# Kernel optimization log

Hardware: AMD Instinct MI355X
Metric: run time of the kernel (lower is better)

The kernel has to match this reference:

```python
import jax, jax.numpy as jnp
import numpy as np

B, Q, K, D, H, HD, HID, ED, CPB, E = 2, 300, 1024, 256, 8, 32, 32, 256, 256, 131072
N = B * Q
EPS = 1e-5


def _ln(x, g, b):
    mu = x.mean(-1, keepdims=True)
    v = ((x - mu) ** 2).mean(-1, keepdims=True)
    return (x - mu) / jnp.sqrt(v + EPS) * g + b


def setup_inputs():
    key = jax.random.key(0)
    ks = jax.random.split(key, 32)
    rn = lambda k, s, sc=0.02: jax.random.normal(k, s, jnp.float32) * sc
    return {
        "nodes": jax.random.normal(ks[0], (N, D), jnp.float32),
        "images": jax.random.normal(ks[1], (B, K, D), jnp.float32),
        "rel_coords": jax.random.normal(ks[2], (B, Q, K, 2), jnp.float32),
        "edge_feats": jax.random.normal(ks[3], (E, ED), jnp.float32),
        "edge_index": jax.random.randint(ks[4], (2, E), 0, N, jnp.int32),
        "images_mask": jnp.zeros((B, K), dtype=bool),
        "ln1_g": jnp.ones((D,)), "ln1_b": jnp.zeros((D,)),
        "ln2_g": jnp.ones((D,)), "ln2_b": jnp.zeros((D,)),
        "ln3_g": jnp.ones((D,)), "ln3_b": jnp.zeros((D,)),
        "Wni": rn(ks[5], (D, HID * H)), "bni": jnp.zeros((HID * H,)),
        "Wnj": rn(ks[6], (D, HID * H)), "bnj": jnp.zeros((HID * H,)),
        "We": rn(ks[7], (ED, HID * H)), "be": jnp.zeros((HID * H,)),
        "attn_proj": jax.random.normal(ks[8], (H, HID), jnp.float32),
        "Wmsg": rn(ks[9], (D + ED, D)), "bmsg": jnp.zeros((D,)),
        "Wg_out": rn(ks[10], (D, D)), "bg_out": jnp.zeros((D,)),
        "Wq": rn(ks[11], (D, D)), "bq": jnp.zeros((D,)),
        "Wkv": rn(ks[12], (D, 2 * D)), "bkv": jnp.zeros((2 * D,)),
        "Wc1": rn(ks[13], (2, CPB), 0.5), "bc1": jnp.zeros((CPB,)),
        "Wc2": rn(ks[14], (CPB, H), 0.1), "bc2": jnp.zeros((H,)),
        "Wc_out": rn(ks[15], (D, D)), "bc_out": jnp.zeros((D,)),
        "Wf1": rn(ks[16], (D, 4 * D)), "bf1": jnp.zeros((4 * D,)),
        "Wf2": rn(ks[17], (4 * D, D)), "bf2": jnp.zeros((D,)),
    }


def reference(nodes, images, rel_coords, edge_feats, edge_index, images_mask,
              ln1_g, ln1_b, ln2_g, ln2_b, ln3_g, ln3_b,
              Wni, bni, Wnj, bnj, We, be, attn_proj, Wmsg, bmsg, Wg_out, bg_out,
              Wq, bq, Wkv, bkv, Wc1, bc1, Wc2, bc2, Wc_out, bc_out,
              Wf1, bf1, Wf2, bf2):
    src, dst = edge_index[0], edge_index[1]
    # --- graph attention (pre-LN residual) ---
    x = _ln(nodes, ln1_g, ln1_b)
    ni, nj = x[src], x[dst]  # [E, D]
    hidden = jax.nn.leaky_relu(
        ni @ Wni + bni + nj @ Wnj + bnj + edge_feats @ We + be, 0.2)
    hidden = hidden.reshape(E, H, HID)
    logits = jnp.einsum('ehd,hd->eh', hidden, attn_proj)  # [E, H]
    m = jax.ops.segment_max(logits, src, num_segments=N)
    z = jnp.exp(logits - m[src])
    scores = z / jax.ops.segment_sum(z, src, num_segments=N)[src]  # scatter softmax
    msg = (jnp.concatenate([nj, edge_feats], -1) @ Wmsg + bmsg).reshape(E, H, HD)
    agg = jax.ops.segment_sum(msg * scores[..., None], src, num_segments=N).reshape(N, D)
    nodes = nodes + (agg @ Wg_out + bg_out)
    # --- cross attention with continuous position bias ---
    x2 = _ln(nodes, ln2_g, ln2_b).reshape(B, Q, D)
    q = (x2 @ Wq + bq).reshape(B, Q, H, HD).transpose(0, 2, 1, 3)  # [B,H,Q,hd]
    kv = (images @ Wkv + bkv).reshape(B, K, 2, H, HD)
    k = kv[:, :, 0].transpose(0, 2, 1, 3)  # [B,H,K,hd]
    v = kv[:, :, 1].transpose(0, 2, 1, 3)
    cpb = jax.nn.relu(rel_coords @ Wc1 + bc1) @ Wc2 + bc2  # [B,Q,K,H]
    bias = jnp.where(images_mask[:, None, None, :], -jnp.inf,
                     jnp.transpose(cpb, (0, 3, 1, 2)))  # [B,H,Q,K]
    att = jnp.einsum('bhqd,bhkd->bhqk', q, k) / jnp.sqrt(jnp.float32(HD)) + bias
    p = jax.nn.softmax(att, axis=-1)
    out = jnp.einsum('bhqk,bhkd->bhqd', p, v)
    out = out.reshape(B, Q, H * HD)  # faithful to original: reshape WITHOUT head transpose
    nodes = nodes + (out @ Wc_out + bc_out).reshape(N, D)
    # --- FFN (residual from the normed input, as in original) ---
    x3 = _ln(nodes, ln3_g, ln3_b)
    ff = jax.nn.gelu(x3 @ Wf1 + bf1, approximate=False) @ Wf2 + bf2
    return ff + x3
```

## Files before the change

kernel.cpp:

```cpp
#include <hip/hip_runtime.h>
#include <hip/hip_bf16.h>
#include <math.h>

#define E_   131072
#define N_   600
#define NB_  2
#define NQ_  300
#define NK_  1024
#define NH_  8

typedef __hip_bfloat16 bf16;
typedef __bf16 bh8 __attribute__((ext_vector_type(8)));
typedef float  fx4 __attribute__((ext_vector_type(4)));

static __device__ __forceinline__ float b2f(bf16 x){ return __bfloat162float(x); }
static __device__ __forceinline__ unsigned short bfu(float x){
  return __bfloat16_as_ushort(__float2bfloat16(x));
}
static __device__ __forceinline__ unsigned pack2(float x, float y){
  return (unsigned)bfu(x) | ((unsigned)bfu(y) << 16);
}
static __device__ __forceinline__ float ldf(const void* p, size_t i, bool isf32){
  return isf32 ? ((const float*)p)[i] : b2f(((const bf16*)p)[i]);
}

constexpr int WOFF[32] = {
  0,256,512,768,1024,1280,
  1536,67072,67328,132864,
  133120,133376,
  133632,264704,
  264960,330496,330752,396288,
  396544,527616,
  528128,528640,528896,530944,
  530952,596488,
  596744,858888,859912,1122056,
  1122312,
  1187848};
#define NWSEG 31
#define WTOT  1187848
struct SrcTab { const void* p[NWSEG]; };
struct TrTab { int4 d[8]; };

static __device__ __forceinline__ void ln_stats(float v, int t, float* r1, float* r2,
                                                float& mu, float& rstd){
  float s1 = v, s2 = v*v;
  #pragma unroll
  for (int o = 32; o; o >>= 1){ s1 += __shfl_down(s1, o); s2 += __shfl_down(s2, o); }
  if ((t & 63) == 0){ r1[t>>6] = s1; r2[t>>6] = s2; }
  __syncthreads();
  float t1 = r1[0]+r1[1]+r1[2]+r1[3];
  float t2 = r2[0]+r2[1]+r2[2]+r2[3];
  mu = t1 * (1.f/256.f);
  float var = t2 * (1.f/256.f) - mu*mu;
  rstd = rsqrtf(var + 1e-5f);
  __syncthreads();
}

__global__ void k_init(int* cnt, float* denom, const void* nodes, int* dflag){
  int i = blockIdx.x*256 + threadIdx.x;
  if (i < N_) cnt[i] = 0;
  if (i < N_*NH_) denom[i] = 0.f;
  if (i == 0){
    const unsigned short* h = (const unsigned short*)nodes;
    int odd = 0;
    for (int j = 0; j < 64; j++){
      int e = (h[j] >> 7) & 0xFF;
      if (e < 100 || e > 150) odd++;
    }
    *dflag = (odd > 8) ? 1 : 0;
  }
}

__global__ __launch_bounds__(256) void k_cvt(SrcTab tab, float* wall, const int* dflag){
  int i = blockIdx.x*256 + threadIdx.x;
  if (i >= WTOT) return;
  bool isf32 = (*dflag != 0);
  int seg = 0;
  while (seg < NWSEG-1 && i >= WOFF[seg+1]) seg++;
  wall[i] = ldf(tab.p[seg], (size_t)(i - WOFF[seg]), isf32);
}

__global__ __launch_bounds__(256) void k_tr(TrTab tab, const float* __restrict__ wall,
                                            bf16* __restrict__ wbt)
{
  __shared__ float tile[64][65];
  int4 d = tab.d[blockIdx.z];
  int K = d.y, Nn = d.z;
  int k0 = blockIdx.x*64, n0 = blockIdx.y*64;
  if (k0 >= K || n0 >= Nn) return;
  const float* src = wall + d.x;
  bf16* dst = wbt + d.w;
  int t = threadIdx.x;
  int rr = t >> 6, cc = t & 63;
  #pragma unroll
  for (int p = 0; p < 16; p++){
    int row = p*4 + rr;
    tile[row][cc] = src[(size_t)(k0 + row)*Nn + n0 + cc];
  }
  __syncthreads();
  #pragma unroll
  for (int p = 0; p < 16; p++){
    int row = p*4 + rr;
    dst[(size_t)(n0 + row)*K + k0 + cc] = __float2bfloat16(tile[cc][row]);
  }
}

__global__ __launch_bounds__(256) void k_ln1(
    const void* __restrict__ nodes, const int* __restrict__ dflag,
    const float* __restrict__ g1, const float* __restrict__ b1, bf16* __restrict__ x1)
{
  __shared__ float r1[4], r2[4];
  int n = blockIdx.x, t = threadIdx.x;
  bool isf32 = (*dflag != 0);
  float v = ldf(nodes, (size_t)n*256 + t, isf32);
  float mu, rstd;
  ln_stats(v, t, r1, r2, mu, rstd);
  x1[n*256 + t] = __float2bfloat16((v - mu) * rstd * g1[t] + b1[t]);
}

__global__ void k_count(const int* __restrict__ ei, int* cnt){
  int e = blockIdx.x*256 + threadIdx.x;
  atomicAdd(&cnt[ei[e]], 1);
}

__global__ __launch_bounds__(1024) void k_scan(const int* __restrict__ cnt,
                                               int* offs, int* cursor){
  __shared__ int s[1024];
  int t = threadIdx.x;
  s[t] = (t < N_) ? cnt[t] : 0;
  __syncthreads();
  for (int o = 1; o < 1024; o <<= 1){
    int v = 0;
    if (t >= o) v = s[t - o];
    __syncthreads();
    if (t >= o) s[t] += v;
    __syncthreads();
  }
  if (t < N_){ int excl = (t == 0) ? 0 : s[t-1]; offs[t] = excl; cursor[t] = excl; }
  if (t == N_-1) offs[N_] = s[N_-1];
}

__global__ void k_scatter(const int* __restrict__ ei, int* cursor, int* eorder){
  int e = blockIdx.x*256 + threadIdx.x;
  int pos = atomicAdd(&cursor[ei[e]], 1);
  eorder[pos] = e;
}

__global__ __launch_bounds__(256) void k_gemm_dual(
    const void* __restrict__ A, int m_base, const int* __restrict__ dflag,
    const bf16* __restrict__ BT, bf16* __restrict__ C)
{
  __shared__ __align__(16) bf16 As[128*40];
  __shared__ __align__(16) bf16 Bs[128*40];
  int m0 = blockIdx.x * 128;
  int n0 = blockIdx.y * 128;
  int t = threadIdx.x;
  bool isf32 = (*dflag != 0);
  int wave = t >> 6, lane = t & 63;
  int wr = (wave >> 1) * 64, wc = (wave & 1) * 64;
  int lm = lane & 15, lq = lane >> 4;
  int srow = t >> 2;
  int scol = (t & 3) * 8;
  size_t r0 = (size_t)(m_base + m0 + srow) * 256;
  size_t r1 = (size_t)(m_base + m0 + 64 + srow) * 256;
  fx4 acc[4][4] = {};
  for (int kk = 0; kk < 256; kk += 32){
    uint4 pa0, pa1;
    if (isf32){
      const float* a0p = (const float*)A + r0 + kk + scol;
      const float* a1p = (const float*)A + r1 + kk + scol;
      float4 va0a = *(const float4*)(a0p);
      float4 va0b = *(const float4*)(a0p + 4);
      float4 va1a = *(const float4*)(a1p);
      float4 va1b = *(const float4*)(a1p + 4);
      pa0.x = pack2(va0a.x, va0a.y); pa0.y = pack2(va0a.z, va0a.w);
      pa0.z = pack2(va0b.x, va0b.y); pa0.w = pack2(va0b.z, va0b.w);
      pa1.x = pack2(va1a.x, va1a.y); pa1.y = pack2(va1a.z, va1a.w);
      pa1.z = pack2(va1b.x, va1b.y); pa1.w = pack2(va1b.z, va1b.w);
    } else {
      pa0 = *(const uint4*)((const bf16*)A + r0 + kk + scol);
      pa1 = *(const uint4*)((const bf16*)A + r1 + kk + scol);
    }
    float4 vb0 = *(const float4*)(BT + (size_t)(n0 + srow)      * 256 + kk + scol);
    float4 vb1 = *(const float4*)(BT + (size_t)(n0 + 64 + srow) * 256 + kk + scol);
    __syncthreads();
    *(uint4*)(As + srow*40 + scol)         = pa0;
    *(uint4*)(As + (64 + srow)*40 + scol)  = pa1;
    *(float4*)(Bs + srow*40 + scol)        = vb0;
    *(float4*)(Bs + (64 + srow)*40 + scol) = vb1;
    __syncthreads();
    bh8 af[4], bfr[4];
    #pragma unroll
    for (int mt = 0; mt < 4; mt++)
      af[mt] = *reinterpret_cast<const bh8*>(As + (wr + mt*16 + lm)*40 + lq*8);
    #pragma unroll
    for (int nt = 0; nt < 4; nt++)
      bfr[nt] = *reinterpret_cast<const bh8*>(Bs + (wc + nt*16 + lm)*40 + lq*8);
    #pragma unroll
    for (int mt = 0; mt < 4; mt++)
      #pragma unroll
      for (int nt = 0; nt < 4; nt++)
        acc[mt][nt] = __builtin_amdgcn_mfma_f32_16x16x32_bf16(af[mt], bfr[nt], acc[mt][nt], 0, 0, 0);
  }
  #pragma unroll
  for (int mt = 0; mt < 4; mt++)
    #pragma unroll
    for (int nt = 0; nt < 4; nt++)
      #pragma unroll
      for (int r = 0; r < 4; r++){
        int row = m0 + wr + mt*16 + lq*4 + r;
        int col = n0 + wc + nt*16 + lm;
        C[(size_t)row*256 + col] = __float2bfloat16(acc[mt][nt][r]);
      }
}

__global__ __launch_bounds__(256) void k_gemm(
    const void* __restrict__ A, const int* __restrict__ dflag, int adual,
    int K, int M, const bf16* __restrict__ BT, int mode,
    void* __restrict__ D, int ldd,
    const float* __restrict__ bias, const float* __restrict__ add,
    float* __restrict__ aux)
{
  __shared__ __align__(16) bf16 As[128*40];
  __shared__ __align__(16) bf16 Bs[128*40];
  int m0 = blockIdx.x * 128;
  int n0 = blockIdx.y * 128;
  int t = threadIdx.x;
  bool f32src = adual && (*dflag != 0);
  int wave = t >> 6, lane = t & 63;
  int wr = (wave >> 1) * 64, wc = (wave & 1) * 64;
  int lm = lane & 15, lq = lane >> 4;
  int srow = t >> 2;
  int scol = (t & 3) * 8;
  size_t rA0 = (size_t)(m0 + srow) * K;
  size_t rA1 = (size_t)(m0 + 64 + srow) * K;
  size_t rB0 = (size_t)(n0 + srow) * K;
  size_t rB1 = (size_t)(n0 + 64 + srow) * K;
  fx4 acc[4][4] = {};
  for (int kk = 0; kk < K; kk += 32){
    uint4 pa0, pa1;
    if (f32src){
      const float* a0p = (const float*)A + rA0 + kk + scol;
      const float* a1p = (const float*)A + rA1 + kk + scol;
      float4 a = *(const float4*)(a0p), b = *(const float4*)(a0p + 4);
      float4 c = *(const float4*)(a1p), d = *(const float4*)(a1p + 4);
      pa0.x = pack2(a.x,a.y); pa0.y = pack2(a.z,a.w);
      pa0.z = pack2(b.x,b.y); pa0.w = pack2(b.z,b.w);
      pa1.x = pack2(c.x,c.y); pa1.y = pack2(c.z,c.w);
      pa1.z = pack2(d.x,d.y); pa1.w = pack2(d.z,d.w);
    } else {
      pa0 = *(const uint4*)((const bf16*)A + rA0 + kk + scol);
      pa1 = *(const uint4*)((const bf16*)A + rA1 + kk + scol);
    }
    float4 vb0 = *(const float4*)(BT + rB0 + kk + scol);
    float4 vb1 = *(const float4*)(BT + rB1 + kk + scol);
    __syncthreads();
    *(uint4*)(As + srow*40 + scol)         = pa0;
    *(uint4*)(As + (64 + srow)*40 + scol)  = pa1;
    *(float4*)(Bs + srow*40 + scol)        = vb0;
    *(float4*)(Bs + (64 + srow)*40 + scol) = vb1;
    __syncthreads();
    bh8 af[4], bfr[4];
    #pragma unroll
    for (int mt = 0; mt < 4; mt++)
      af[mt] = *reinterpret_cast<const bh8*>(As + (wr + mt*16 + lm)*40 + lq*8);
    #pragma unroll
    for (int nt = 0; nt < 4; nt++)
      bfr[nt] = *reinterpret_cast<const bh8*>(Bs + (wc + nt*16 + lm)*40 + lq*8);
    #pragma unroll
    for (int mt = 0; mt < 4; mt++)
      #pragma unroll
      for (int nt = 0; nt < 4; nt++)
        acc[mt][nt] = __builtin_amdgcn_mfma_f32_16x16x32_bf16(af[mt], bfr[nt], acc[mt][nt], 0, 0, 0);
  }
  #pragma unroll
  for (int mt = 0; mt < 4; mt++)
    #pragma unroll
    for (int nt = 0; nt < 4; nt++)
      #pragma unroll
      for (int r = 0; r < 4; r++){
        int row = m0 + wr + mt*16 + lq*4 + r;
        int col = n0 + wc + nt*16 + lm;
        if (row >= M) continue;
        float v = acc[mt][nt][r];
        if (mode == 0){
          if (bias) v += bias[col];
          ((float*)D)[(size_t)row*ldd + col] = v;
        } else if (mode == 1){
          v += bias[col];
          if (col < 256){
            ((float*)D)[(size_t)row*256 + col] = v;
          } else {
            int b = row >> 10, ki = row & 1023;
            int hh = (col - 256) >> 5, dd = (col - 256) & 31;
            aux[(((size_t)b*NH_ + hh)*32 + dd)*NK_ + ki] = v;
          }
        } else if (mode == 2){
          v += bias[col] + add[(size_t)row*ldd + col];
          ((float*)D)[(size_t)row*ldd + col] = v;
        } else {
          v += bias[col];
          float g = 0.5f*v*(1.f + erff(v*0.70710678118654752f));
          ((bf16*)D)[(size_t)row*ldd + col] = __float2bfloat16(g);
        }
      }
}

__global__ __launch_bounds__(256) void k_logits(
    const bf16* __restrict__ He, const float* __restrict__ Pall,
    const float* __restrict__ bni, const float* __restrict__ bnj, const float* __restrict__ be,
    const float* __restrict__ ap, const int* __restrict__ ei,
    float* __restrict__ z, float* __restrict__ denom, int e0chunk)
{
  __shared__ float hs[32*264];
  __shared__ int   ssh[32], dsh[32];
  __shared__ float aps[256], bhs[256];
  int t = threadIdx.x;
  int base = e0chunk + blockIdx.x*32;
  if (t < 32) ssh[t] = ei[base + t];
  else if (t < 64) dsh[t-32] = ei[E_ + base + (t - 32)];
  aps[t] = ap[t];
  bhs[t] = bni[t] + bnj[t] + be[t];
  __syncthreads();
  int slot = (t >> 5)*33 + (t & 31);
  for (int r = 0; r < 32; r++){
    float v = b2f(He[(size_t)(base - e0chunk + r)*256 + t])
            + Pall[ssh[r]*768 + t] + Pall[dsh[r]*768 + 256 + t] + bhs[t];
    v = (v > 0.f) ? v : 0.2f*v;
    hs[r*264 + slot] = v;
  }
  __syncthreads();
  int e = t >> 3, h = t & 7;
  const float* hr  = hs + e*264 + h*33;
  const float* apr = aps + h*32;
  float acc = 0.f;
  #pragma unroll
  for (int i = 0; i < 32; i++) acc = fmaf(hr[i], apr[i], acc);
  float zv = __expf(fminf(acc, 30.f));
  z[(size_t)(base + e)*8 + h] = zv;
  atomicAdd(&denom[ssh[e]*8 + h], zv);
}

__global__ __launch_bounds__(256) void k_agg_e(
    const int* __restrict__ offs, const int* __restrict__ eorder, const int* __restrict__ ei,
    const float* __restrict__ z,
    const void* __restrict__ ef, const int* __restrict__ dflag,
    const float* __restrict__ Pall,
    float* __restrict__ Fbuf, float* __restrict__ Gbuf)
{
  __shared__ float zsh[32*8];
  __shared__ int   esh[32];
  __shared__ int   dsh[32];
  int n = blockIdx.x, s = blockIdx.y, t = threadIdx.x;
  bool isf32 = (*dflag != 0);
  int h = t >> 5;
  int e0 = offs[n], e1 = offs[n+1];
  int total = e1 - e0;
  int quarter = (total + 3) >> 2;
  int start = e0 + s*quarter;
  int end   = min(e1, start + quarter);
  float facc[8] = {};
  float gacc = 0.f;
  int jz = t >> 3, hz = t & 7;
  for (int base = start; base < end; base += 32){
    int cnt = min(32, end - base);
    __syncthreads();
    if (t < 32){
      int e = (t < cnt) ? eorder[base + t] : eorder[start];
      esh[t] = e;
      dsh[t] = ei[E_ + e];
    }
    __syncthreads();
    zsh[t] = (jz < cnt) ? z[(size_t)esh[jz]*8 + hz] : 0.f;
    __syncthreads();
    #pragma unroll 8
    for (int jj = 0; jj < 32; jj++){
      int e = esh[jj];
      float efv = ldf(ef, (size_t)e*256 + t, isf32);
      float pv  = Pall[(size_t)dsh[jj]*768 + 512 + t];
      #pragma unroll
      for (int hq = 0; hq < 8; hq++) facc[hq] = fmaf(zsh[jj*8 + hq], efv, facc[hq]);
      gacc = fmaf(zsh[jj*8 + h], pv, gacc);
    }
  }
  int slot = n*4 + s;
  #pragma unroll
  for (int hq = 0; hq < 8; hq++)
    Fbuf[((size_t)slot*8 + hq)*256 + t] = facc[hq];
  Gbuf[(size_t)slot*256 + t] = gacc;
}

__global__ __launch_bounds__(256) void k_agg_n(
    const float* __restrict__ Fbuf, const float* __restrict__ Gbuf,
    const float* __restrict__ denom,
    const float* __restrict__ bmsg, const float* __restrict__ Wmsg,
    const void* __restrict__ nodes, const int* __restrict__ dflag,
    const float* __restrict__ Wg, const float* __restrict__ bg,
    const float* __restrict__ g2, const float* __restrict__ b2v,
    const float* __restrict__ Wq, const float* __restrict__ bq,
    float* __restrict__ nodes1, float* __restrict__ qbuf)
{
  __shared__ float sinv[8];
  __shared__ float Fs[8*257];
  __shared__ float aggs[256];
  __shared__ float r1[4], r2[4];
  int n = blockIdx.x, t = threadIdx.x;
  bool isf32 = (*dflag != 0);
  int h = t >> 5;
  if (t < 8){
    float dsum = denom[n*8 + t];
    sinv[t] = (dsum > 0.f) ? 1.f/dsum : 0.f;
  }
  __syncthreads();
  #pragma unroll
  for (int hq = 0; hq < 8; hq++){
    float f = 0.f;
    #pragma unroll
    for (int s = 0; s < 4; s++)
      f += Fbuf[((size_t)(n*4 + s)*8 + hq)*256 + t];
    Fs[hq*257 + t] = f * sinv[hq];
  }
  float gacc = 0.f;
  #pragma unroll
  for (int s = 0; s < 4; s++) gacc += Gbuf[(size_t)(n*4 + s)*256 + t];
  gacc *= sinv[h];
  __syncthreads();
  float am = gacc + bmsg[t];
  const float* fr = Fs + h*257;
  for (int k = 0; k < 256; k++)
    am = fmaf(fr[k], Wmsg[(size_t)(256 + k)*256 + t], am);
  aggs[t] = am;
  __syncthreads();
  float o = bg[t] + ldf(nodes, (size_t)n*256 + t, isf32);
  for (int k = 0; k < 256; k++) o = fmaf(aggs[k], Wg[k*256 + t], o);
  nodes1[n*256 + t] = o;
  float mu, rstd;
  ln_stats(o, t, r1, r2, mu, rstd);
  float x2 = (o - mu) * rstd * g2[t] + b2v[t];
  __syncthreads();
  aggs[t] = x2;
  __syncthreads();
  float q = bq[t];
  for (int k = 0; k < 256; k++) q = fmaf(aggs[k], Wq[k*256 + t], q);
  qbuf[n*256 + t] = q;
}

__global__ __launch_bounds__(256) void k_cpb(
    const void* __restrict__ rel, const int* __restrict__ dflag,
    const float* __restrict__ Wc1, const float* __restrict__ bc1,
    const float* __restrict__ Wc2, const float* __restrict__ bc2, bf16* __restrict__ bias)
{
  __shared__ float w0[256], w1[256], bb[256], w2[256*8], b2s[8];
  int t = threadIdx.x;
  bool isf32 = (*dflag != 0);
  w0[t] = Wc1[t]; w1[t] = Wc1[256 + t]; bb[t] = bc1[t];
  for (int i = t; i < 2048; i += 256) w2[i] = Wc2[i];
  if (t < 8) b2s[t] = bc2[t];
  __syncthreads();
  size_t pos = (size_t)blockIdx.x*256 + t;
  float c0 = ldf(rel, pos*2, isf32), c1 = ldf(rel, pos*2 + 1, isf32);
  float acc[8] = {};
  for (int j = 0; j < 256; j++){
    float hj = fmaf(c0, w0[j], fmaf(c1, w1[j], bb[j]));
    hj = fmaxf(hj, 0.f);
    #pragma unroll
    for (int h = 0; h < 8; h++) acc[h] = fmaf(hj, w2[j*8 + h], acc[h]);
  }
  int k = (int)(pos & 1023);
  size_t qq = pos >> 10;
  size_t b = qq / NQ_, q = qq % NQ_;
  bf16* dst = bias + ((b*NH_)*NQ_ + q)*NK_;
  #pragma unroll
  for (int h = 0; h < 8; h++)
    dst[(size_t)h*NQ_*NK_ + k] = __float2bfloat16(acc[h] + b2s[h]);
}

__global__ __launch_bounds__(256) void k_attn(
    const float* __restrict__ qbuf, const float* __restrict__ kbuf, const float* __restrict__ vT,
    const bf16* __restrict__ bias, bf16* __restrict__ Yb)
{
  __shared__ float Qs[8*33];
  __shared__ float Ks[128*33];
  __shared__ float Sc[8*1024];
  __shared__ float Op[4*8*32];
  __shared__ float qs[8];
  int qt = blockIdx.x, h = blockIdx.y, b = blockIdx.z;
  int q0 = qt*8;
  int t = threadIdx.x;
  {
    int q = t >> 5, d = t & 31;
    int gq = q0 + q;
    Qs[q*33 + d] = (gq < NQ_) ? qbuf[((size_t)b*NQ_ + gq)*256 + h*32 + d] : 0.f;
  }
  const float* kbase = kbuf + (size_t)b*NK_*256 + h*32;
  const bf16*  bb    = bias + ((size_t)(b*NH_ + h)*NQ_)*NK_;
  int kl = t & 127;
  int qb = (t >> 7) * 4;
  for (int kt = 0; kt < 8; kt++){
    int k0 = kt*128;
    __syncthreads();
    {
      int r = t >> 1, c0 = (t & 1) * 16;
      const float* src = kbase + (size_t)(k0 + r)*256 + c0;
      float* dst = Ks + r*33 + c0;
      #pragma unroll
      for (int ii = 0; ii < 4; ii++){
        float4 f = *(const float4*)(src + ii*4);
        dst[ii*4+0]=f.x; dst[ii*4+1]=f.y; dst[ii*4+2]=f.z; dst[ii*4+3]=f.w;
      }
    }
    __syncthreads();
    float a0=0.f, a1=0.f, a2=0.f, a3=0.f;
    const float* kr = Ks + kl*33;
    #pragma unroll
    for (int i = 0; i < 32; i++){
      float kd = kr[i];
      a0 = fmaf(kd, Qs[(qb+0)*33+i], a0);
      a1 = fmaf(kd, Qs[(qb+1)*33+i], a1);
      a2 = fmaf(kd, Qs[(qb+2)*33+i], a2);
      a3 = fmaf(kd, Qs[(qb+3)*33+i], a3);
    }
    float av[4] = {a0,a1,a2,a3};
    #pragma unroll
    for (int j = 0; j < 4; j++){
      int gq = min(q0 + qb + j, NQ_-1);
      float s = av[j]*0.17677669529663689f + b2f(bb[(size_t)gq*NK_ + k0 + kl]);
      Sc[(qb+j)*1024 + k0 + kl] = s;
    }
  }
  __syncthreads();
  {
    int q = t >> 5, j = t & 31;
    float m = -1e30f;
    for (int k = j; k < 1024; k += 32) m = fmaxf(m, Sc[q*1024 + k]);
    #pragma unroll
    for (int o = 16; o; o >>= 1) m = fmaxf(m, __shfl_xor(m, o));
    float ssum = 0.f;
    for (int k = j; k < 1024; k += 32){
      float e = __expf(Sc[q*1024 + k] - m);
      Sc[q*1024 + k] = e;
      ssum += e;
    }
    #pragma unroll
    for (int o = 16; o; o >>= 1) ssum += __shfl_xor(ssum, o);
    if (j == 0) qs[q] = ssum;
  }
  int d = t & 31, qg = (t >> 5) & 1, ks = t >> 6;
  const float* vrb = vT + (((size_t)(b*NH_ + h))*32)*NK_;
  float o0=0.f, o1=0.f, o2=0.f, o3=0.f;
  for (int kt = 0; kt < 8; kt++){
    int k0 = kt*128;
    __syncthreads();
    {
      int d2 = t >> 3, kq = (t & 7) * 16;
      const float* src = vrb + (size_t)d2*NK_ + k0 + kq;
      #pragma unroll
      for (int ii = 0; ii < 4; ii++){
        float4 f = *(const float4*)(src + ii*4);
        Ks[(kq+ii*4+0)*33 + d2] = f.x;
        Ks[(kq+ii*4+1)*33 + d2] = f.y;
        Ks[(kq+ii*4+2)*33 + d2] = f.z;
        Ks[(kq+ii*4+3)*33 + d2] = f.w;
      }
    }
    __syncthreads();
    const float* sc0 = Sc + (qg*4+0)*1024 + k0 + ks*32;
    const float* sc1 = Sc + (qg*4+1)*1024 + k0 + ks*32;
    const float* sc2 = Sc + (qg*4+2)*1024 + k0 + ks*32;
    const float* sc3 = Sc + (qg*4+3)*1024 + k0 + ks*32;
    #pragma unroll
    for (int kk = 0; kk < 32; kk++){
      float vv = Ks[(ks*32+kk)*33 + d];
      o0 = fmaf(sc0[kk], vv, o0);
      o1 = fmaf(sc1[kk], vv, o1);
      o2 = fmaf(sc2[kk], vv, o2);
      o3 = fmaf(sc3[kk], vv, o3);
    }
  }
  Op[((ks*8) + qg*4 + 0)*32 + d] = o0;
  Op[((ks*8) + qg*4 + 1)*32 + d] = o1;
  Op[((ks*8) + qg*4 + 2)*32 + d] = o2;
  Op[((ks*8) + qg*4 + 3)*32 + d] = o3;
  __syncthreads();
  {
    int q = t >> 5, dd = t & 31;
    int gq = q0 + q;
    if (gq < NQ_){
      float s = Op[(0*8+q)*32+dd] + Op[(1*8+q)*32+dd]
              + Op[(2*8+q)*32+dd] + Op[(3*8+q)*32+dd];
      float sv = s / qs[q];
      int tt = h*NQ_ + gq;
      Yb[((size_t)b*NQ_ + (tt >> 3))*256 + (tt & 7)*32 + dd] = __float2bfloat16(sv);
    }
  }
}

__global__ __launch_bounds__(256) void k_ln3(
    const float* __restrict__ n2, const float* __restrict__ g3, const float* __restrict__ b3,
    float* __restrict__ x3f, bf16* __restrict__ x3b)
{
  __shared__ float r1[4], r2[4];
  int n = blockIdx.x, t = threadIdx.x;
  float v = n2[n*256 + t];
  float mu, rstd;
  ln_stats(v, t, r1, r2, mu, rstd);
  float x3 = (v - mu) * rstd * g3[t] + b3[t];
  x3f[n*256 + t] = x3;
  x3b[n*256 + t] = __float2bfloat16(x3);
}

extern "C" void kernel_launch(void* const* d_in, const int* in_sizes, int n_in,
                              void* d_out, int out_size, void* d_ws, size_t ws_size,
                              hipStream_t stream)
{
  const void* nodes  = d_in[0];
  const void* images = d_in[1];
  const void* rel    = d_in[2];
  const void* ef     = d_in[3];
  const int*  ei     = (const int*)d_in[4];
  float* out = (float*)d_out;

  char* w = (char*)d_ws;
  auto alloc = [&](size_t bytes) -> void* {
    void* p = (void*)w; w += (bytes + 255) & ~(size_t)255; return p;
  };
  int*      dflag  = (int*)     alloc(4);
  float*    Wall   = (float*)   alloc((size_t)WTOT*4);
  bf16*     Wbt    = (bf16*)    alloc((size_t)983040*2);
  bf16*     bias   = (bf16*)    alloc((size_t)NB_*NH_*NQ_*NK_*2);
  float*    zbuf   = (float*)   alloc((size_t)E_*8*4);
  float*    Pall   = (float*)   alloc((size_t)N_*768*4);
  float*    Fbuf   = (float*)   alloc((size_t)N_*4*8*256*4);
  float*    Gbuf   = (float*)   alloc((size_t)N_*4*256*4);
  float*    nodes1 = (float*)   alloc(N_*256*4);
  float*    qbuf   = (float*)   alloc(N_*256*4);
  float*    kbuf   = (float*)   alloc((size_t)NB_*NK_*256*4);
  float*    vT     = (float*)   alloc((size_t)NB_*NH_*32*NK_*4);
  float*    n2buf  = (float*)   alloc(N_*256*4);
  float*    x3f    = (float*)   alloc(N_*256*4);
  bf16*     x1     = (bf16*)    alloc(N_*256*2);
  bf16*     x3b    = (bf16*)    alloc(N_*256*2);
  bf16*     Yb     = (bf16*)    alloc(N_*256*2);
  bf16*     H1     = (bf16*)    alloc((size_t)N_*1024*2);
  float*    denom  = (float*)   alloc(N_*8*4);
  int*      cnt    = (int*)     alloc(N_*4);
  int*      offs   = (int*)     alloc((N_+1)*4);
  int*      cursor = (int*)     alloc(N_*4);
  int*      eorder = (int*)     alloc((size_t)E_*4);
  size_t used = (size_t)(w - (char*)d_ws);
  int CH = E_;
  while (CH > 2048 && used + (size_t)CH*256*2 + 256 > ws_size) CH >>= 1;
  bf16* He = (bf16*)alloc((size_t)CH*256*2);

  bf16* WeT  = Wbt + 0;
  bf16* WkvT = Wbt + 65536;
  bf16* WnpT = Wbt + 196608;
  bf16* WcoT = Wbt + 393216;
  bf16* Wf1T = Wbt + 458752;
  bf16* Wf2T = Wbt + 720896;

  const float *ln1g=Wall+WOFF[0],  *ln1b=Wall+WOFF[1];
  const float *ln2g=Wall+WOFF[2],  *ln2b=Wall+WOFF[3];
  const float *ln3g=Wall+WOFF[4],  *ln3b=Wall+WOFF[5];
  const float *bni=Wall+WOFF[7],  *bnj=Wall+WOFF[9], *be=Wall+WOFF[10];
  const float *ap =Wall+WOFF[11];
  const float *Wmsg=Wall+WOFF[12], *bmsg=Wall+WOFF[13];
  const float *Wg=Wall+WOFF[14], *bg=Wall+WOFF[15];
  const float *Wq=Wall+WOFF[16], *bq=Wall+WOFF[17];
  const float *bkv=Wall+WOFF[19];
  const float *Wc1=Wall+WOFF[20], *bc1=Wall+WOFF[21];
  const float *Wc2=Wall+WOFF[22], *bc2=Wall+WOFF[23];
  const float *bco=Wall+WOFF[25];
  const float *bf1v=Wall+WOFF[27];
  const float *bf2v=Wall+WOFF[29];

  SrcTab tab;
  {
    const int idx[NWSEG] = {6,7,8,9,10,11, 12,13,14,15, 17,18, 19,20, 21,22,23,24,
                            25,26, 27,28,29,30, 31,32, 33,34,35,36, 16};
    for (int i = 0; i < NWSEG; i++) tab.p[i] = d_in[idx[i]];
  }
  TrTab tr;
  tr.d[0] = {WOFF[30], 256,  256, 0};
  tr.d[1] = {WOFF[18], 256,  512, 65536};
  tr.d[2] = {WOFF[6],  256,  256, 196608};
  tr.d[3] = {WOFF[8],  256,  256, 196608+65536};
  tr.d[4] = {WOFF[12], 256,  256, 196608+131072};
  tr.d[5] = {WOFF[24], 256,  256, 393216};
  tr.d[6] = {WOFF[26], 256, 1024, 458752};
  tr.d[7] = {WOFF[28],1024,  256, 720896};

  k_init   <<<19, 256, 0, stream>>>(cnt, denom, nodes, dflag);
  k_cvt    <<<(WTOT+255)/256, 256, 0, stream>>>(tab, Wall, dflag);
  k_tr     <<<dim3(16,16,8), 256, 0, stream>>>(tr, Wall, Wbt);
  k_ln1    <<<N_, 256, 0, stream>>>(nodes, dflag, ln1g, ln1b, x1);
  k_count  <<<E_/256, 256, 0, stream>>>(ei, cnt);
  k_scan   <<<1, 1024, 0, stream>>>(cnt, offs, cursor);
  k_scatter<<<E_/256, 256, 0, stream>>>(ei, cursor, eorder);

  k_gemm<<<dim3(5,6), 256, 0, stream>>>(x1, dflag, 0, 256, N_, WnpT, 0,
                                        Pall, 768, nullptr, nullptr, nullptr);

  for (int c0 = 0; c0 < E_; c0 += CH){
    k_gemm_dual<<<dim3(CH/128, 2), 256, 0, stream>>>(ef, c0, dflag, WeT, He);
    k_logits   <<<CH/32, 256, 0, stream>>>(He, Pall, bni, bnj, be, ap, ei,
                                           zbuf, denom, c0);
  }
  k_agg_e  <<<dim3(N_,4), 256, 0, stream>>>(offs, eorder, ei, zbuf, ef, dflag, Pall,
                                            Fbuf, Gbuf);
  k_agg_n  <<<N_, 256, 0, stream>>>(Fbuf, Gbuf, denom, bmsg, Wmsg, nodes, dflag,
                                    Wg, bg, ln2g, ln2b, Wq, bq, nodes1, qbuf);
  k_gemm<<<dim3(16,4), 256, 0, stream>>>(images, dflag, 1, 256, NB_*NK_, WkvT, 1,
                                         kbuf, 256, bkv, nullptr, vT);
  k_cpb    <<<NB_*NQ_*NK_/256, 256, 0, stream>>>(rel, dflag, Wc1, bc1, Wc2, bc2, bias);
  dim3 agrid((NQ_ + 7)/8, NH_, NB_);
  k_attn   <<<agrid, 256, 0, stream>>>(qbuf, kbuf, vT, bias, Yb);
  k_gemm<<<dim3(5,2), 256, 0, stream>>>(Yb, dflag, 0, 256, N_, WcoT, 2,
                                        n2buf, 256, bco, nodes1, nullptr);
  k_ln3  <<<N_, 256, 0, stream>>>(n2buf, ln3g, ln3b, x3f, x3b);
  k_gemm<<<dim3(5,8), 256, 0, stream>>>(x3b, dflag, 0, 256, N_, Wf1T, 3,
                                        H1, 1024, bf1v, nullptr, nullptr);
  k_gemm<<<dim3(5,2), 256, 0, stream>>>(H1, dflag, 0, 1024, N_, Wf2T, 2,
                                        out, 256, bf2v, x3f, nullptr);
}
```

Baseline: 730.7 us.

## Fuse edge GEMM with attention logits and software-prefetch next K tile

Merges the edge-feature projection GEMM with the leaky-ReLU/attention-projection logits step into one kernel, so the per-edge hidden tensor is reduced in registers via lane shuffles instead of being written to and reread from a bf16 buffer. The GEMM main loop also issues global loads for the next K slice before the MFMA work on the current one. The epilogue now does scattered Pall gathers per accumulator element and per-block denominator atomics, which adds register pressure and irregular loads inside the GEMM kernel.

```diff
diff --git a/kernel.cpp b/kernel.cpp
--- a/kernel.cpp
+++ b/kernel.cpp
@@ -146,14 +146,20 @@
   eorder[pos] = e;
 }
 
-__global__ __launch_bounds__(256) void k_gemm_dual(
-    const void* __restrict__ A, int m_base, const int* __restrict__ dflag,
-    const bf16* __restrict__ BT, bf16* __restrict__ C)
+__global__ __launch_bounds__(256) void k_he_logits(
+    const void* __restrict__ A, const int* __restrict__ dflag,
+    const bf16* __restrict__ BT, const float* __restrict__ Pall,
+    const float* __restrict__ bni, const float* __restrict__ bnj, const float* __restrict__ be,
+    const float* __restrict__ ap, const int* __restrict__ ei,
+    float* __restrict__ z, float* __restrict__ denom)
 {
   __shared__ __align__(16) bf16 As[128*40];
   __shared__ __align__(16) bf16 Bs[128*40];
-  int m0 = blockIdx.x * 128;
+  __shared__ int ssh[128], dsh[128];
+  __shared__ __align__(16) float zs[128*4];
+  int e0 = blockIdx.x * 128;
   int n0 = blockIdx.y * 128;
+  int gy = blockIdx.y;
   int t = threadIdx.x;
   bool isf32 = (*dflag != 0);
   int wave = t >> 6, lane = t & 63;
@@ -161,34 +167,53 @@
   int lm = lane & 15, lq = lane >> 4;
   int srow = t >> 2;
   int scol = (t & 3) * 8;
-  size_t r0 = (size_t)(m_base + m0 + srow) * 256;
-  size_t r1 = (size_t)(m_base + m0 + 64 + srow) * 256;
+
+  if (t < 128) ssh[t] = ei[e0 + t];
+  else         dsh[t-128] = ei[E_ + e0 + (t-128)];
+
+  size_t rA0 = (size_t)(e0 + srow) * 256;
+  size_t rA1 = (size_t)(e0 + 64 + srow) * 256;
+  size_t rB0 = (size_t)(n0 + srow) * 256;
+  size_t rB1 = (size_t)(n0 + 64 + srow) * 256;
+
   fx4 acc[4][4] = {};
+  float4 fa0, fa1, fa2, fa3;
+  uint4  ba0, ba1;
+  float4 fb0, fb1;
+
+  auto issue = [&](int kk){
+    if (isf32){
+      const float* p0 = (const float*)A + rA0 + kk + scol;
+      const float* p1 = (const float*)A + rA1 + kk + scol;
+      fa0 = *(const float4*)p0;  fa1 = *(const float4*)(p0 + 4);
+      fa2 = *(const float4*)p1;  fa3 = *(const float4*)(p1 + 4);
+    } else {
+      ba0 = *(const uint4*)((const bf16*)A + rA0 + kk + scol);
+      ba1 = *(const uint4*)((const bf16*)A + rA1 + kk + scol);
+    }
+    fb0 = *(const float4*)(BT + rB0 + kk + scol);
+    fb1 = *(const float4*)(BT + rB1 + kk + scol);
+  };
+  auto commit = [&](){
+    uint4 w0, w1;
+    if (isf32){
+      w0.x = pack2(fa0.x, fa0.y); w0.y = pack2(fa0.z, fa0.w);
+      w0.z = pack2(fa1.x, fa1.y); w0.w = pack2(fa1.z, fa1.w);
+      w1.x = pack2(fa2.x, fa2.y); w1.y = pack2(fa2.z, fa2.w);
+      w1.z = pack2(fa3.x, fa3.y); w1.w = pack2(fa3.z, fa3.w);
+    } else { w0 = ba0; w1 = ba1; }
+    *(uint4*)(As + srow*40 + scol)         = w0;
+    *(uint4*)(As + (64 + srow)*40 + scol)  = w1;
+    *(float4*)(Bs + srow*40 + scol)        = fb0;
+    *(float4*)(Bs + (64 + srow)*40 + scol) = fb1;
+  };
+
+  issue(0);
   for (int kk = 0; kk < 256; kk += 32){
-    uint4 pa0, pa1;
-    if (isf32){
-      const float* a0p = (const float*)A + r0 + kk + scol;
-      const float* a1p = (const float*)A + r1 + kk + scol;
-      float4 va0a = *(const float4*)(a0p);
-      float4 va0b = *(const float4*)(a0p + 4);
-      float4 va1a = *(const float4*)(a1p);
-      float4 va1b = *(const float4*)(a1p + 4);
-      pa0.x = pack2(va0a.x, va0a.y); pa0.y = pack2(va0a.z, va0a.w);
-      pa0.z = pack2(va0b.x, va0b.y); pa0.w = pack2(va0b.z, va0b.w);
-      pa1.x = pack2(va1a.x, va1a.y); pa1.y = pack2(va1a.z, va1a.w);
-      pa1.z = pack2(va1b.x, va1b.y); pa1.w = pack2(va1b.z, va1b.w);
-    } else {
-      pa0 = *(const uint4*)((const bf16*)A + r0 + kk + scol);
-      pa1 = *(const uint4*)((const bf16*)A + r1 + kk + scol);
-    }
-    float4 vb0 = *(const float4*)(BT + (size_t)(n0 + srow)      * 256 + kk + scol);
-    float4 vb1 = *(const float4*)(BT + (size_t)(n0 + 64 + srow) * 256 + kk + scol);
-    __syncthreads();
-    *(uint4*)(As + srow*40 + scol)         = pa0;
-    *(uint4*)(As + (64 + srow)*40 + scol)  = pa1;
-    *(float4*)(Bs + srow*40 + scol)        = vb0;
-    *(float4*)(Bs + (64 + srow)*40 + scol) = vb1;
-    __syncthreads();
+    __syncthreads();
+    commit();
+    __syncthreads();
+    if (kk < 224) issue(kk + 32);
     bh8 af[4], bfr[4];
     #pragma unroll
     for (int mt = 0; mt < 4; mt++)
@@ -202,16 +227,51 @@
       for (int nt = 0; nt < 4; nt++)
         acc[mt][nt] = __builtin_amdgcn_mfma_f32_16x16x32_bf16(af[mt], bfr[nt], acc[mt][nt], 0, 0, 0);
   }
-  #pragma unroll
-  for (int mt = 0; mt < 4; mt++)
-    #pragma unroll
-    for (int nt = 0; nt < 4; nt++)
+
+  float apc[4], bhc[4];
+  #pragma unroll
+  for (int nt = 0; nt < 4; nt++){
+    int c = n0 + wc + nt*16 + lm;
+    apc[nt] = ap[c];
+    bhc[nt] = bni[c] + bnj[c] + be[c];
+  }
+  #pragma unroll
+  for (int mt = 0; mt < 4; mt++){
+    #pragma unroll
+    for (int r = 0; r < 4; r++){
+      int eL = wr + mt*16 + lq*4 + r;
+      int sn = ssh[eL], dn = dsh[eL];
+      float l0 = 0.f, l1 = 0.f;
       #pragma unroll
-      for (int r = 0; r < 4; r++){
-        int row = m0 + wr + mt*16 + lq*4 + r;
-        int col = n0 + wc + nt*16 + lm;
-        C[(size_t)row*256 + col] = __float2bfloat16(acc[mt][nt][r]);
+      for (int nt = 0; nt < 4; nt++){
+        int c = n0 + wc + nt*16 + lm;
+        float v = acc[mt][nt][r]
+                + Pall[(size_t)sn*768 + c]
+                + Pall[(size_t)dn*768 + 256 + c] + bhc[nt];
+        v = (v > 0.f) ? v : 0.2f*v;
+        float pv = v * apc[nt];
+        if (nt < 2) l0 += pv; else l1 += pv;
       }
+      #pragma unroll
+      for (int o = 8; o; o >>= 1){ l0 += __shfl_xor(l0, o); l1 += __shfl_xor(l1, o); }
+      if (lm == 0){
+        zs[eL*4 + (wc >> 5) + 0] = __expf(fminf(l0, 30.f));
+        zs[eL*4 + (wc >> 5) + 1] = __expf(fminf(l1, 30.f));
+      }
+    }
+  }
+  __syncthreads();
+  {
+    int e = t >> 1, half = t & 1;
+    float2 vv = *(const float2*)&zs[e*4 + half*2];
+    *(float2*)&z[(size_t)(e0 + e)*8 + gy*4 + half*2] = vv;
+  }
+  #pragma unroll
+  for (int i = 0; i < 2; i++){
+    int idx = t*2 + i;
+    int ee = idx >> 2, hh = idx & 3;
+    atomicAdd(&denom[ssh[ee]*8 + gy*4 + hh], zs[ee*4 + hh]);
+  }
 }
 
 __global__ __launch_bounds__(256) void k_gemm(
@@ -306,41 +366,6 @@
       }
 }
 
-__global__ __launch_bounds__(256) void k_logits(
-    const bf16* __restrict__ He, const float* __restrict__ Pall,
-    const float* __restrict__ bni, const float* __restrict__ bnj, const float* __restrict__ be,
-    const float* __restrict__ ap, const int* __restrict__ ei,
-    float* __restrict__ z, float* __restrict__ denom, int e0chunk)
-{
-  __shared__ float hs[32*264];
-  __shared__ int   ssh[32], dsh[32];
-  __shared__ float aps[256], bhs[256];
-  int t = threadIdx.x;
-  int base = e0chunk + blockIdx.x*32;
-  if (t < 32) ssh[t] = ei[base + t];
-  else if (t < 64) dsh[t-32] = ei[E_ + base + (t - 32)];
-  aps[t] = ap[t];
-  bhs[t] = bni[t] + bnj[t] + be[t];
-  __syncthreads();
-  int slot = (t >> 5)*33 + (t & 31);
-  for (int r = 0; r < 32; r++){
-    float v = b2f(He[(size_t)(base - e0chunk + r)*256 + t])
-            + Pall[ssh[r]*768 + t] + Pall[dsh[r]*768 + 256 + t] + bhs[t];
-    v = (v > 0.f) ? v : 0.2f*v;
-    hs[r*264 + slot] = v;
-  }
-  __syncthreads();
-  int e = t >> 3, h = t & 7;
-  const float* hr  = hs + e*264 + h*33;
-  const float* apr = aps + h*32;
-  float acc = 0.f;
-  #pragma unroll
-  for (int i = 0; i < 32; i++) acc = fmaf(hr[i], apr[i], acc);
-  float zv = __expf(fminf(acc, 30.f));
-  z[(size_t)(base + e)*8 + h] = zv;
-  atomicAdd(&denom[ssh[e]*8 + h], zv);
-}
-
 __global__ __launch_bounds__(256) void k_agg_e(
     const int* __restrict__ offs, const int* __restrict__ eorder, const int* __restrict__ ei,
     const float* __restrict__ z,
@@ -647,10 +672,6 @@
   int*      offs   = (int*)     alloc((N_+1)*4);
   int*      cursor = (int*)     alloc(N_*4);
   int*      eorder = (int*)     alloc((size_t)E_*4);
-  size_t used = (size_t)(w - (char*)d_ws);
-  int CH = E_;
-  while (CH > 2048 && used + (size_t)CH*256*2 + 256 > ws_size) CH >>= 1;
-  bf16* He = (bf16*)alloc((size_t)CH*256*2);
 
   bf16* WeT  = Wbt + 0;
   bf16* WkvT = Wbt + 65536;
@@ -701,11 +722,9 @@
   k_gemm<<<dim3(5,6), 256, 0, stream>>>(x1, dflag, 0, 256, N_, WnpT, 0,
                                         Pall, 768, nullptr, nullptr, nullptr);
 
-  for (int c0 = 0; c0 < E_; c0 += CH){
-    k_gemm_dual<<<dim3(CH/128, 2), 256, 0, stream>>>(ef, c0, dflag, WeT, He);
-    k_logits   <<<CH/32, 256, 0, stream>>>(He, Pall, bni, bnj, be, ap, ei,
-                                           zbuf, denom, c0);
-  }
+  k_he_logits<<<dim3(E_/128, 2), 256, 0, stream>>>(ef, dflag, WeT, Pall,
+                                                   bni, bnj, be, ap, ei, zbuf, denom);
+
   k_agg_e  <<<dim3(N_,4), 256, 0, stream>>>(offs, eorder, ei, zbuf, ef, dflag, Pall,
                                             Fbuf, Gbuf);
   k_agg_n  <<<N_, 256, 0, stream>>>(Fbuf, Gbuf, denom, bmsg, Wmsg, nodes, dflag,
```

New measurement: 743.5 us. Within noise of the previous version (+1.8%).

## Fuse edge aggregation with node projection kernel, drop split-K partial buffers

Applied to the files above, without the earlier changes.

Merges the edge-aggregation kernel (previously split four ways per node) and the node-level matvec/LN/Q-projection kernel into one kernel with one block per node. This removes the Fbuf/Gbuf partial-sum round trip through global memory and one launch. The cost is fewer blocks (600 instead of 2400) for the edge loop, so each block walks all of its node's edges serially, which can hurt parallelism for nodes with many edges. It also splits the matvec accumulators four ways for ILP and vectorizes the rel_coords load in the cpb kernel.

```diff
diff --git a/kernel.cpp b/kernel.cpp
--- a/kernel.cpp
+++ b/kernel.cpp
@@ -14,6 +14,9 @@
 typedef float  fx4 __attribute__((ext_vector_type(4)));
 
 static __device__ __forceinline__ float b2f(bf16 x){ return __bfloat162float(x); }
+static __device__ __forceinline__ float bfbits2f(unsigned short u){
+  return __uint_as_float((unsigned)u << 16);
+}
 static __device__ __forceinline__ unsigned short bfu(float x){
   return __bfloat16_as_ushort(__float2bfloat16(x));
 }
@@ -341,32 +344,37 @@
   atomicAdd(&denom[ssh[e]*8 + h], zv);
 }
 
-__global__ __launch_bounds__(256) void k_agg_e(
+__global__ __launch_bounds__(256) void k_agg(
     const int* __restrict__ offs, const int* __restrict__ eorder, const int* __restrict__ ei,
     const float* __restrict__ z,
     const void* __restrict__ ef, const int* __restrict__ dflag,
-    const float* __restrict__ Pall,
-    float* __restrict__ Fbuf, float* __restrict__ Gbuf)
+    const float* __restrict__ Pall, const float* __restrict__ denom,
+    const float* __restrict__ bmsg, const float* __restrict__ Wmsg,
+    const void* __restrict__ nodes,
+    const float* __restrict__ Wg, const float* __restrict__ bg,
+    const float* __restrict__ g2, const float* __restrict__ b2v,
+    const float* __restrict__ Wq, const float* __restrict__ bq,
+    float* __restrict__ nodes1, float* __restrict__ qbuf)
 {
   __shared__ float zsh[32*8];
   __shared__ int   esh[32];
   __shared__ int   dsh[32];
-  int n = blockIdx.x, s = blockIdx.y, t = threadIdx.x;
+  __shared__ float Fs[8*257];
+  __shared__ float aggs[256];
+  __shared__ float sinv[8];
+  __shared__ float r1[4], r2[4];
+  int n = blockIdx.x, t = threadIdx.x;
   bool isf32 = (*dflag != 0);
   int h = t >> 5;
   int e0 = offs[n], e1 = offs[n+1];
-  int total = e1 - e0;
-  int quarter = (total + 3) >> 2;
-  int start = e0 + s*quarter;
-  int end   = min(e1, start + quarter);
   float facc[8] = {};
   float gacc = 0.f;
   int jz = t >> 3, hz = t & 7;
-  for (int base = start; base < end; base += 32){
-    int cnt = min(32, end - base);
+  for (int base = e0; base < e1; base += 32){
+    int cnt = min(32, e1 - base);
     __syncthreads();
     if (t < 32){
-      int e = (t < cnt) ? eorder[base + t] : eorder[start];
+      int e = (t < cnt) ? eorder[base + t] : eorder[e0];
       esh[t] = e;
       dsh[t] = ei[E_ + e];
     }
@@ -383,65 +391,57 @@
       gacc = fmaf(zsh[jj*8 + h], pv, gacc);
     }
   }
-  int slot = n*4 + s;
+  if (t < 8){
+    float ds = denom[n*8 + t];
+    sinv[t] = (ds > 0.f) ? 1.f/ds : 0.f;
+  }
+  __syncthreads();
   #pragma unroll
   for (int hq = 0; hq < 8; hq++)
-    Fbuf[((size_t)slot*8 + hq)*256 + t] = facc[hq];
-  Gbuf[(size_t)slot*256 + t] = gacc;
-}
-
-__global__ __launch_bounds__(256) void k_agg_n(
-    const float* __restrict__ Fbuf, const float* __restrict__ Gbuf,
-    const float* __restrict__ denom,
-    const float* __restrict__ bmsg, const float* __restrict__ Wmsg,
-    const void* __restrict__ nodes, const int* __restrict__ dflag,
-    const float* __restrict__ Wg, const float* __restrict__ bg,
-    const float* __restrict__ g2, const float* __restrict__ b2v,
-    const float* __restrict__ Wq, const float* __restrict__ bq,
-    float* __restrict__ nodes1, float* __restrict__ qbuf)
-{
-  __shared__ float sinv[8];
-  __shared__ float Fs[8*257];
-  __shared__ float aggs[256];
-  __shared__ float r1[4], r2[4];
-  int n = blockIdx.x, t = threadIdx.x;
-  bool isf32 = (*dflag != 0);
-  int h = t >> 5;
-  if (t < 8){
-    float dsum = denom[n*8 + t];
-    sinv[t] = (dsum > 0.f) ? 1.f/dsum : 0.f;
-  }
-  __syncthreads();
-  #pragma unroll
-  for (int hq = 0; hq < 8; hq++){
-    float f = 0.f;
-    #pragma unroll
-    for (int s = 0; s < 4; s++)
-      f += Fbuf[((size_t)(n*4 + s)*8 + hq)*256 + t];
-    Fs[hq*257 + t] = f * sinv[hq];
-  }
-  float gacc = 0.f;
-  #pragma unroll
-  for (int s = 0; s < 4; s++) gacc += Gbuf[(size_t)(n*4 + s)*256 + t];
-  gacc *= sinv[h];
-  __syncthreads();
-  float am = gacc + bmsg[t];
+    Fs[hq*257 + t] = facc[hq] * sinv[hq];
+  __syncthreads();
+  float am = gacc * sinv[h] + bmsg[t];
   const float* fr = Fs + h*257;
-  for (int k = 0; k < 256; k++)
-    am = fmaf(fr[k], Wmsg[(size_t)(256 + k)*256 + t], am);
+  {
+    float p0=0.f, p1=0.f, p2=0.f, p3=0.f;
+    for (int k = 0; k < 256; k += 4){
+      p0 = fmaf(fr[k+0], Wmsg[(size_t)(256 + k + 0)*256 + t], p0);
+      p1 = fmaf(fr[k+1], Wmsg[(size_t)(256 + k + 1)*256 + t], p1);
+      p2 = fmaf(fr[k+2], Wmsg[(size_t)(256 + k + 2)*256 + t], p2);
+      p3 = fmaf(fr[k+3], Wmsg[(size_t)(256 + k + 3)*256 + t], p3);
+    }
+    am += (p0 + p1) + (p2 + p3);
+  }
   aggs[t] = am;
   __syncthreads();
   float o = bg[t] + ldf(nodes, (size_t)n*256 + t, isf32);
-  for (int k = 0; k < 256; k++) o = fmaf(aggs[k], Wg[k*256 + t], o);
+  {
+    float p0=0.f, p1=0.f, p2=0.f, p3=0.f;
+    for (int k = 0; k < 256; k += 4){
+      p0 = fmaf(aggs[k+0], Wg[(k+0)*256 + t], p0);
+      p1 = fmaf(aggs[k+1], Wg[(k+1)*256 + t], p1);
+      p2 = fmaf(aggs[k+2], Wg[(k+2)*256 + t], p2);
+      p3 = fmaf(aggs[k+3], Wg[(k+3)*256 + t], p3);
+    }
+    o += (p0 + p1) + (p2 + p3);
+  }
   nodes1[n*256 + t] = o;
   float mu, rstd;
   ln_stats(o, t, r1, r2, mu, rstd);
   float x2 = (o - mu) * rstd * g2[t] + b2v[t];
-  __syncthreads();
   aggs[t] = x2;
   __syncthreads();
   float q = bq[t];
-  for (int k = 0; k < 256; k++) q = fmaf(aggs[k], Wq[k*256 + t], q);
+  {
+    float p0=0.f, p1=0.f, p2=0.f, p3=0.f;
+    for (int k = 0; k < 256; k += 4){
+      p0 = fmaf(aggs[k+0], Wq[(k+0)*256 + t], p0);
+      p1 = fmaf(aggs[k+1], Wq[(k+1)*256 + t], p1);
+      p2 = fmaf(aggs[k+2], Wq[(k+2)*256 + t], p2);
+      p3 = fmaf(aggs[k+3], Wq[(k+3)*256 + t], p3);
+    }
+    q += (p0 + p1) + (p2 + p3);
+  }
   qbuf[n*256 + t] = q;
 }
 
@@ -458,7 +458,15 @@
   if (t < 8) b2s[t] = bc2[t];
   __syncthreads();
   size_t pos = (size_t)blockIdx.x*256 + t;
-  float c0 = ldf(rel, pos*2, isf32), c1 = ldf(rel, pos*2 + 1, isf32);
+  float c0, c1;
+  if (isf32){
+    float2 v = ((const float2*)rel)[pos];
+    c0 = v.x; c1 = v.y;
+  } else {
+    unsigned v = ((const unsigned*)rel)[pos];
+    c0 = bfbits2f((unsigned short)(v & 0xffff));
+    c1 = bfbits2f((unsigned short)(v >> 16));
+  }
   float acc[8] = {};
   for (int j = 0; j < 256; j++){
     float hj = fmaf(c0, w0[j], fmaf(c1, w1[j], bb[j]));
@@ -630,8 +638,6 @@
   bf16*     bias   = (bf16*)    alloc((size_t)NB_*NH_*NQ_*NK_*2);
   float*    zbuf   = (float*)   alloc((size_t)E_*8*4);
   float*    Pall   = (float*)   alloc((size_t)N_*768*4);
-  float*    Fbuf   = (float*)   alloc((size_t)N_*4*8*256*4);
-  float*    Gbuf   = (float*)   alloc((size_t)N_*4*256*4);
   float*    nodes1 = (float*)   alloc(N_*256*4);
   float*    qbuf   = (float*)   alloc(N_*256*4);
   float*    kbuf   = (float*)   alloc((size_t)NB_*NK_*256*4);
@@ -706,10 +712,9 @@
     k_logits   <<<CH/32, 256, 0, stream>>>(He, Pall, bni, bnj, be, ap, ei,
                                            zbuf, denom, c0);
   }
-  k_agg_e  <<<dim3(N_,4), 256, 0, stream>>>(offs, eorder, ei, zbuf, ef, dflag, Pall,
-                                            Fbuf, Gbuf);
-  k_agg_n  <<<N_, 256, 0, stream>>>(Fbuf, Gbuf, denom, bmsg, Wmsg, nodes, dflag,
-                                    Wg, bg, ln2g, ln2b, Wq, bq, nodes1, qbuf);
+  k_agg  <<<N_, 256, 0, stream>>>(offs, eorder, ei, zbuf, ef, dflag, Pall, denom,
+                                  bmsg, Wmsg, nodes, Wg, bg, ln2g, ln2b, Wq, bq,
+                                  nodes1, qbuf);
   k_gemm<<<dim3(16,4), 256, 0, stream>>>(images, dflag, 1, 256, NB_*NK_, WkvT, 1,
                                          kbuf, 256, bkv, nullptr, vT);
   k_cpb    <<<NB_*NQ_*NK_/256, 256, 0, stream>>>(rel, dflag, Wc1, bc1, Wc2, bc2, bias);
```

New measurement: 724.5 us. No clear change (-0.8%).
